# Kernel optimization log

Measured on AMD Instinct MI355X. Metric: run time of the kernel, lower is better.

## Reference

```python
import jax, jax.numpy as jnp
import numpy as np

N_NODES = 100000
N_EDGES = 1600000
IN = 128
HID = 128
EPS = 1e-5


def setup_inputs() -> dict:
    key = jax.random.key(0)
    ks = jax.random.split(key, 20)
    def lin(k, fi, fo):
        return jax.random.normal(k, (fi, fo), dtype=jnp.float32) / np.sqrt(fi)
    inp = {
        'x': jax.random.normal(ks[0], (N_NODES, IN), dtype=jnp.float32),
        'src': jax.random.randint(ks[1], (N_EDGES,), 0, N_NODES),
        'dst': jax.random.randint(ks[2], (N_EDGES,), 0, N_NODES),
        # SAGEConv layer 1..3: fc_self, fc_neigh, bias
        'Wself1': lin(ks[3], IN, HID), 'Wneigh1': lin(ks[4], IN, HID), 'b1': jnp.zeros((HID,), jnp.float32),
        'Wself2': lin(ks[5], HID, HID), 'Wneigh2': lin(ks[6], HID, HID), 'b2': jnp.zeros((HID,), jnp.float32),
        'Wself3': lin(ks[7], HID, HID), 'Wneigh3': lin(ks[8], HID, HID), 'b3': jnp.zeros((HID,), jnp.float32),
        # shared BatchNorm1d(hid)
        'gamma': jnp.ones((HID,), jnp.float32), 'beta': jnp.zeros((HID,), jnp.float32),
        # decoder MLP hid->hid->hid->1
        'Wd1': lin(ks[9], HID, HID), 'bd1': jnp.zeros((HID,), jnp.float32),
        'Wd2': lin(ks[10], HID, HID), 'bd2': jnp.zeros((HID,), jnp.float32),
        'Wd3': lin(ks[11], HID, 1), 'bd3': jnp.zeros((1,), jnp.float32),
    }
    return inp


def _sage_conv(h, src, dst, deg, Wself, Wneigh, b, n):
    # mean aggregation over in-neighbors: gather + segment-sum + divide
    neigh_sum = jax.ops.segment_sum(h[src], dst, num_segments=n)  # [N, F]
    neigh_mean = neigh_sum / deg[:, None]
    return h @ Wself + neigh_mean @ Wneigh + b


def _batch_norm(h, gamma, beta):
    mu = jnp.mean(h, axis=0)
    var = jnp.mean(jnp.square(h - mu), axis=0)  # biased var, as torch BN training
    return gamma * (h - mu) * jax.lax.rsqrt(var + EPS) + beta


def reference(x, src, dst, Wself1, Wneigh1, b1, Wself2, Wneigh2, b2,
              Wself3, Wneigh3, b3, gamma, beta, Wd1, bd1, Wd2, bd2, Wd3, bd3):
    n = x.shape[0]
    deg = jax.ops.segment_sum(jnp.ones_like(dst, dtype=x.dtype), dst, num_segments=n)
    deg = jnp.maximum(deg, 1.0)
    h = _sage_conv(x, src, dst, deg, Wself1, Wneigh1, b1, n)
    h = jax.nn.relu(_batch_norm(h, gamma, beta))  # dropout = identity (eval)
    h = _sage_conv(h, src, dst, deg, Wself2, Wneigh2, b2, n)
    h = jax.nn.relu(_batch_norm(h, gamma, beta))
    h = _sage_conv(h, src, dst, deg, Wself3, Wneigh3, b3, n)
    # decoder MLP
    h = jax.nn.relu(h @ Wd1 + bd1)
    h = jax.nn.relu(h @ Wd2 + bd2)
    return h @ Wd3 + bd3  # [N, 1]
```

## Files before the change

kernel.cpp:

```cpp
#include <hip/hip_runtime.h>

typedef unsigned short u16;
typedef unsigned int u32;
using bf16x8 = __attribute__((ext_vector_type(8))) __bf16;
using f32x4  = __attribute__((ext_vector_type(4))) float;

#define CAP 48
#define LDSROW 136

__global__ void SAGE_79328045957727_kernel() {}

__device__ __forceinline__ float bf2f(u16 u) {
  union { u32 i; float f; } v; v.i = ((u32)u) << 16; return v.f;
}
__device__ __forceinline__ u16 f2bf(float f) {
  union { float f; u32 i; } v; v.f = f;
  u32 x = v.i;
  return (u16)((x + 0x7FFFu + ((x >> 16) & 1u)) >> 16);
}


__global__ void zero_kernel(int* p, int n) {
  int i = blockIdx.x * 256 + threadIdx.x;
  if (i < n) p[i] = 0;
}


__global__ __launch_bounds__(256) void build_kernel(
    const int* __restrict__ src, const int* __restrict__ dst,
    int* __restrict__ deg, int* __restrict__ csr, int E, int npart,
    const float* __restrict__ x, u16* __restrict__ xb, long nelem4,
    const float* w0, const float* w1, const float* w2, const float* w3,
    const float* w4, const float* w5, const float* w6, const float* w7,
    u16* __restrict__ wt) {
  int b = blockIdx.x;
  if (b < 2048) {
    int p = b & 7;
    int brank = b >> 3;
    int lo = p * npart, hi = lo + npart;
    for (int i = brank * 256 + threadIdx.x; i < E; i += 256 * 256) {
      int dv = dst[i];
      if (dv >= lo && dv < hi) {
        int pos = atomicAdd(&deg[dv], 1);
        if (pos < CAP) csr[(size_t)dv * CAP + pos] = src[i];
      }
    }
  } else if (b < 2304) {
    long t = (long)(b - 2048) * 256 + threadIdx.x;
    for (long i4 = t; i4 < nelem4; i4 += 256 * 256) {
      float4 v = ((const float4*)x)[i4];
      u32* op = (u32*)(xb + i4 * 4);
      op[0] = ((u32)f2bf(v.y) << 16) | (u32)f2bf(v.x);
      op[1] = ((u32)f2bf(v.w) << 16) | (u32)f2bf(v.z);
    }
  } else {
    int tg = (b - 2304) * 256 + threadIdx.x;
    for (int k = 0; k < 8; ++k) {
      int idx = tg + k * 16384;
      int m = idx >> 14;
      int i = idx & 16383;
      const float* W = m == 0 ? w0 : m == 1 ? w1 : m == 2 ? w2 : m == 3 ? w3
                     : m == 4 ? w4 : m == 5 ? w5 : m == 6 ? w6 : w7;
      int r = i >> 7, c = i & 127;
      wt[(size_t)m * 16384 + (size_t)c * 128 + r] = f2bf(W[i]);
    }
  }
}


__global__ __launch_bounds__(256) void bnrelu_kernel(
    const u16* __restrict__ Z, u16* __restrict__ G,
    const float* __restrict__ stats, const float* __restrict__ gamma,
    const float* __restrict__ beta, long n4, float invN) {
  __shared__ float sSc[128], sSh[128];
  int t = threadIdx.x;
  if (t < 128) {
    float mu = stats[t] * invN;
    float var = stats[128 + t] * invN - mu * mu;
    float is = rsqrtf(var + 1e-5f);
    float sc = gamma[t] * is;
    sSc[t] = sc;
    sSh[t] = beta[t] - mu * sc;
  }
  __syncthreads();
  for (long i4 = (long)blockIdx.x * 256 + t; i4 < n4; i4 += (long)gridDim.x * 256) {
    uint4 q = ((const uint4*)Z)[i4];
    int c0 = ((int)(i4 & 15)) * 8;
    float e0 = fmaxf(sSc[c0+0]*bf2f((u16)(q.x & 0xffffu))+sSh[c0+0], 0.f);
    float e1 = fmaxf(sSc[c0+1]*bf2f((u16)(q.x >> 16))    +sSh[c0+1], 0.f);
    float e2 = fmaxf(sSc[c0+2]*bf2f((u16)(q.y & 0xffffu))+sSh[c0+2], 0.f);
    float e3 = fmaxf(sSc[c0+3]*bf2f((u16)(q.y >> 16))    +sSh[c0+3], 0.f);
    float e4 = fmaxf(sSc[c0+4]*bf2f((u16)(q.z & 0xffffu))+sSh[c0+4], 0.f);
    float e5 = fmaxf(sSc[c0+5]*bf2f((u16)(q.z >> 16))    +sSh[c0+5], 0.f);
    float e6 = fmaxf(sSc[c0+6]*bf2f((u16)(q.w & 0xffffu))+sSh[c0+6], 0.f);
    float e7 = fmaxf(sSc[c0+7]*bf2f((u16)(q.w >> 16))    +sSh[c0+7], 0.f);
    uint4 o;
    o.x = ((u32)f2bf(e1) << 16) | (u32)f2bf(e0);
    o.y = ((u32)f2bf(e3) << 16) | (u32)f2bf(e2);
    o.z = ((u32)f2bf(e5) << 16) | (u32)f2bf(e4);
    o.w = ((u32)f2bf(e7) << 16) | (u32)f2bf(e6);
    ((uint4*)G)[i4] = o;
  }
}


__global__ __launch_bounds__(256) void gather_kernel(
    const u16* __restrict__ G, const int* __restrict__ csr,
    const int* __restrict__ deg, u16* __restrict__ M, int N) {
  int node = blockIdx.x * 16 + (threadIdx.x >> 4);
  if (node >= N) return;
  int lane = threadIdx.x & 15;
  int fo = lane * 8;
  const int* nl = csr + (size_t)node * CAP;
  int d = deg[node];
  int dm = d < CAP ? d : CAP;
  float a0=0.f,a1=0.f,a2=0.f,a3=0.f,a4=0.f,a5=0.f,a6=0.f,a7=0.f;

#define ACC8(q) do { \
    a0 += bf2f((u16)((q).x & 0xffffu)); a1 += bf2f((u16)((q).x >> 16)); \
    a2 += bf2f((u16)((q).y & 0xffffu)); a3 += bf2f((u16)((q).y >> 16)); \
    a4 += bf2f((u16)((q).z & 0xffffu)); a5 += bf2f((u16)((q).z >> 16)); \
    a6 += bf2f((u16)((q).w & 0xffffu)); a7 += bf2f((u16)((q).w >> 16)); \
  } while (0)

  int e = 0;
  for (; e + 8 <= dm; e += 8) {
    int ia = nl[e+0], ib = nl[e+1], ic = nl[e+2], id_ = nl[e+3];
    int ie_ = nl[e+4], if_ = nl[e+5], ig = nl[e+6], ih = nl[e+7];
    uint4 q0 = *(const uint4*)(G + (size_t)ia  * 128 + fo);
    uint4 q1 = *(const uint4*)(G + (size_t)ib  * 128 + fo);
    uint4 q2 = *(const uint4*)(G + (size_t)ic  * 128 + fo);
    uint4 q3 = *(const uint4*)(G + (size_t)id_ * 128 + fo);
    uint4 q4 = *(const uint4*)(G + (size_t)ie_ * 128 + fo);
    uint4 q5 = *(const uint4*)(G + (size_t)if_ * 128 + fo);
    uint4 q6 = *(const uint4*)(G + (size_t)ig  * 128 + fo);
    uint4 q7 = *(const uint4*)(G + (size_t)ih  * 128 + fo);
    ACC8(q0); ACC8(q1); ACC8(q2); ACC8(q3);
    ACC8(q4); ACC8(q5); ACC8(q6); ACC8(q7);
  }
  if (e + 4 <= dm) {
    int ia = nl[e+0], ib = nl[e+1], ic = nl[e+2], id_ = nl[e+3];
    uint4 q0 = *(const uint4*)(G + (size_t)ia  * 128 + fo);
    uint4 q1 = *(const uint4*)(G + (size_t)ib  * 128 + fo);
    uint4 q2 = *(const uint4*)(G + (size_t)ic  * 128 + fo);
    uint4 q3 = *(const uint4*)(G + (size_t)id_ * 128 + fo);
    ACC8(q0); ACC8(q1); ACC8(q2); ACC8(q3);
    e += 4;
  }
  for (; e < dm; ++e) {
    uint4 q = *(const uint4*)(G + (size_t)nl[e] * 128 + fo);
    ACC8(q);
  }
#undef ACC8

  float inv = 1.f / (float)(d > 0 ? d : 1);
  uint4 o;
  o.x = ((u32)f2bf(a1 * inv) << 16) | (u32)f2bf(a0 * inv);
  o.y = ((u32)f2bf(a3 * inv) << 16) | (u32)f2bf(a2 * inv);
  o.z = ((u32)f2bf(a5 * inv) << 16) | (u32)f2bf(a4 * inv);
  o.w = ((u32)f2bf(a7 * inv) << 16) | (u32)f2bf(a6 * inv);
  *(uint4*)(M + (size_t)node * 128 + fo) = o;
}


__device__ __forceinline__ void stage_tile(
    const u16* __restrict__ A, u16* sT, size_t row0, int N, int tid) {
  for (int j = 0; j < 8; ++j) {
    int idx = j * 1024 + tid * 4;
    int r = idx >> 6;
    int c = idx & 63;
    size_t grow = row0 + r;
    if (grow >= (size_t)N) grow = (size_t)(N - 1);
    const u32* gp = (const u32*)(A + grow * 128) + c;
    u32 v0 = gp[0], v1 = gp[1], v2 = gp[2], v3 = gp[3];
    u32* lp = (u32*)(sT + (size_t)r * LDSROW + c * 2);
    lp[0] = v0; lp[1] = v1; lp[2] = v2; lp[3] = v3;
  }
}

__device__ __forceinline__ void mfma_tile(
    const u16* sT, const u16* __restrict__ Wt, f32x4 acc[8][2],
    int wave, int l15, int quad) {
  bf16x8 wf[2][4];
  for (int ct = 0; ct < 2; ++ct) {
    int col = wave * 32 + ct * 16 + l15;
    for (int kk = 0; kk < 4; ++kk)
      wf[ct][kk] = *(const bf16x8*)(Wt + (size_t)col * 128 + kk * 32 + quad * 8);
  }
  for (int kk = 0; kk < 4; ++kk) {
    int kbase = kk * 32 + quad * 8;
    for (int rt = 0; rt < 8; ++rt) {
      bf16x8 af = *(const bf16x8*)(sT + (size_t)(rt * 16 + l15) * LDSROW + kbase);
      acc[rt][0] = __builtin_amdgcn_mfma_f32_16x16x32_bf16(af, wf[0][kk], acc[rt][0], 0, 0, 0);
      acc[rt][1] = __builtin_amdgcn_mfma_f32_16x16x32_bf16(af, wf[1][kk], acc[rt][1], 0, 0, 0);
    }
  }
}


__global__ __launch_bounds__(256) void gemm2(
    const u16* __restrict__ A, const u16* __restrict__ B,
    const u16* __restrict__ W1t, const u16* __restrict__ W2t,
    const float* __restrict__ bias, u16* __restrict__ C,
    float* __restrict__ statsOut, int N) {
  __shared__ u16 sT[128 * LDSROW];
  int tid = threadIdx.x;
  int wave = tid >> 6;
  int lane = tid & 63;
  int l15 = lane & 15;
  int quad = lane >> 4;
  size_t row0 = (size_t)blockIdx.x * 128;

  f32x4 acc[8][2];
  for (int rt = 0; rt < 8; ++rt)
    for (int ct = 0; ct < 2; ++ct)
      for (int i = 0; i < 4; ++i) acc[rt][ct][i] = 0.f;

  stage_tile(A, sT, row0, N, tid);
  __syncthreads();
  mfma_tile(sT, W1t, acc, wave, l15, quad);
  __syncthreads();
  stage_tile(B, sT, row0, N, tid);
  __syncthreads();
  mfma_tile(sT, W2t, acc, wave, l15, quad);

  for (int ct = 0; ct < 2; ++ct) {
    int col = wave * 32 + ct * 16 + l15;
    float bv = bias[col];
    float ssum = 0.f, ssq = 0.f;
    for (int rt = 0; rt < 8; ++rt) {
      for (int i = 0; i < 4; ++i) {
        size_t row = row0 + rt * 16 + quad * 4 + i;
        if (row < (size_t)N) {
          float v = acc[rt][ct][i] + bv;
          C[row * 128 + col] = f2bf(v);
          ssum += v; ssq += v * v;
        }
      }
    }
    for (int o = 16; o < 64; o <<= 1) {
      ssum += __shfl_xor(ssum, o);
      ssq  += __shfl_xor(ssq, o);
    }
    if (quad == 0) {
      atomicAdd(&statsOut[col], ssum);
      atomicAdd(&statsOut[128 + col], ssq);
    }
  }
}


__global__ __launch_bounds__(256) void megagemm(
    const u16* __restrict__ G, const u16* __restrict__ M,
    const u16* __restrict__ wtS3, const u16* __restrict__ wtN3,
    const float* __restrict__ b3,
    const u16* __restrict__ wtD1, const float* __restrict__ bd1,
    const u16* __restrict__ wtD2, const float* __restrict__ bd2,
    const float* __restrict__ wd3, const float* __restrict__ bd3,
    float* __restrict__ outF, int N) {
  __shared__ u16 sT[128 * LDSROW];
  __shared__ float sOut[128];

  int tid = threadIdx.x;
  int wave = tid >> 6;
  int lane = tid & 63;
  int l15 = lane & 15;
  int quad = lane >> 4;
  size_t row0 = (size_t)blockIdx.x * 128;

  if (tid < 128) sOut[tid] = 0.f;

  f32x4 acc[8][2];
  for (int rt = 0; rt < 8; ++rt)
    for (int ct = 0; ct < 2; ++ct)
      for (int i = 0; i < 4; ++i) acc[rt][ct][i] = 0.f;

  stage_tile(M, sT, row0, N, tid);
  __syncthreads();
  mfma_tile(sT, wtN3, acc, wave, l15, quad);
  __syncthreads();
  stage_tile(G, sT, row0, N, tid);
  __syncthreads();
  mfma_tile(sT, wtS3, acc, wave, l15, quad);

  for (int g = 0; g < 2; ++g) {
    const u16* Wt = g ? wtD2 : wtD1;
    const float* bs = g ? bd1 : b3;
    int do_relu = g;

    __syncthreads();
    for (int ct = 0; ct < 2; ++ct) {
      int col = wave * 32 + ct * 16 + l15;
      float bv = bs[col];
      for (int rt = 0; rt < 8; ++rt) {
        for (int i = 0; i < 4; ++i) {
          int row = rt * 16 + quad * 4 + i;
          float v = acc[rt][ct][i] + bv;
          if (do_relu) v = fmaxf(v, 0.f);
          sT[(size_t)row * LDSROW + col] = f2bf(v);
        }
      }
    }
    __syncthreads();

    for (int rt = 0; rt < 8; ++rt)
      for (int ct = 0; ct < 2; ++ct)
        for (int i = 0; i < 4; ++i) acc[rt][ct][i] = 0.f;
    mfma_tile(sT, Wt, acc, wave, l15, quad);
  }

  {
    int col0 = wave * 32 + l15;
    float bv0 = bd2[col0], bv1 = bd2[col0 + 16];
    float w30 = wd3[col0], w31 = wd3[col0 + 16];
    for (int rt = 0; rt < 8; ++rt) {
      for (int i = 0; i < 4; ++i) {
        size_t row = row0 + rt * 16 + quad * 4 + i;
        float v0 = fmaxf(acc[rt][0][i] + bv0, 0.f);
        float v1 = fmaxf(acc[rt][1][i] + bv1, 0.f);
        float pv = v0 * w30 + v1 * w31;
        pv += __shfl_xor(pv, 1);
        pv += __shfl_xor(pv, 2);
        pv += __shfl_xor(pv, 4);
        pv += __shfl_xor(pv, 8);
        if (l15 == 0 && row < (size_t)N)
          atomicAdd(&sOut[rt * 16 + quad * 4 + i], pv);
      }
    }
    __syncthreads();
    if (tid < 128) {
      size_t row = row0 + tid;
      if (row < (size_t)N) outF[row] = sOut[tid] + bd3[0];
    }
  }
}


extern "C" void kernel_launch(void* const* d_in, const int* in_sizes, int n_in,
                              void* d_out, int out_size, void* d_ws, size_t ws_size,
                              hipStream_t stream) {
  const float* x      = (const float*)d_in[0];
  const int*   src    = (const int*)d_in[1];
  const int*   dst    = (const int*)d_in[2];
  const float* Wself1 = (const float*)d_in[3];
  const float* Wneigh1= (const float*)d_in[4];
  const float* b1     = (const float*)d_in[5];
  const float* Wself2 = (const float*)d_in[6];
  const float* Wneigh2= (const float*)d_in[7];
  const float* b2     = (const float*)d_in[8];
  const float* Wself3 = (const float*)d_in[9];
  const float* Wneigh3= (const float*)d_in[10];
  const float* b3     = (const float*)d_in[11];
  const float* gamma  = (const float*)d_in[12];
  const float* beta   = (const float*)d_in[13];
  const float* Wd1    = (const float*)d_in[14];
  const float* bd1    = (const float*)d_in[15];
  const float* Wd2    = (const float*)d_in[16];
  const float* bd2    = (const float*)d_in[17];
  const float* Wd3    = (const float*)d_in[18];
  const float* bd3    = (const float*)d_in[19];
  float* out = (float*)d_out;

  int N = in_sizes[0] / 128;
  int E = in_sizes[1];
  int npart = (N + 7) / 8;

  char* ws = (char*)d_ws;
  size_t off = 0;
  int* deg; int* csr; float* stats1; float* stats2;
  u16* xb; u16* ZA; u16* ZB; u16* M; u16* wt;
  deg   = (int*)(ws + off);   off += (size_t)N * 4;
  stats1= (float*)(ws + off); off += 256 * 4;
  stats2= (float*)(ws + off); off += 256 * 4;
  off = (off + 511) & ~(size_t)511;
  csr  = (int*)(ws + off);   off += ((size_t)N * CAP * 4 + 511) & ~(size_t)511;
  wt   = (u16*)(ws + off);   off += ((size_t)8 * 16384 * 2 + 511) & ~(size_t)511;
  xb   = (u16*)(ws + off);   off += ((size_t)N * 128 * 2 + 511) & ~(size_t)511;
  ZA   = (u16*)(ws + off);   off += ((size_t)N * 128 * 2 + 511) & ~(size_t)511;
  ZB   = (u16*)(ws + off);   off += ((size_t)N * 128 * 2 + 511) & ~(size_t)511;
  M    = (u16*)(ws + off);   off += ((size_t)N * 128 * 2 + 511) & ~(size_t)511;

  u16* wtS1 = wt + 0 * 16384; u16* wtN1 = wt + 1 * 16384;
  u16* wtS2 = wt + 2 * 16384; u16* wtN2 = wt + 3 * 16384;
  u16* wtS3 = wt + 4 * 16384; u16* wtN3 = wt + 5 * 16384;
  u16* wtD1 = wt + 6 * 16384; u16* wtD2 = wt + 7 * 16384;

  zero_kernel<<<(N + 512 + 255) / 256, 256, 0, stream>>>(deg, N + 512);

  long nelem4 = (long)N * 128 / 4;
  build_kernel<<<2368, 256, 0, stream>>>(
      src, dst, deg, csr, E, npart, x, xb, nelem4,
      Wself1, Wneigh1, Wself2, Wneigh2, Wself3, Wneigh3, Wd1, Wd2, wt);

  int strips = (N + 127) / 128;
  int g16    = (N + 15) / 16;
  float invN = 1.f / (float)N;
  long n4 = (long)N * 16;

  gather_kernel<<<g16, 256, 0, stream>>>(xb, csr, deg, M, N);
  gemm2<<<strips, 256, 0, stream>>>(xb, M, wtS1, wtN1, b1, ZA, stats1, N);

  bnrelu_kernel<<<2048, 256, 0, stream>>>(ZA, ZA, stats1, gamma, beta, n4, invN);

  gather_kernel<<<g16, 256, 0, stream>>>(ZA, csr, deg, M, N);
  gemm2<<<strips, 256, 0, stream>>>(ZA, M, wtS2, wtN2, b2, ZB, stats2, N);

  bnrelu_kernel<<<2048, 256, 0, stream>>>(ZB, ZB, stats2, gamma, beta, n4, invN);

  gather_kernel<<<g16, 256, 0, stream>>>(ZB, csr, deg, M, N);
  megagemm<<<strips, 256, 0, stream>>>(
      ZB, M, wtS3, wtN3, b3, wtD1, bd1, wtD2, bd2, Wd3, bd3, out, N);
}
```

Before: 564.8 us.

## Prefetch second GEMM operand into registers and simplify CSR build partitioning

The two-operand GEMM kernels now load the second input tile into registers before the first MFMA pass, so its global reads overlap with compute instead of being issued after a barrier. The CSR build no longer makes 8 partitioned passes over the edge list that each filter by destination range. Every edge is now handled once with an atomic insert, which cuts redundant reads of dst but gives up the partition's locality of atomics. The register prefetch adds 32 VGPRs per thread, which may lower occupancy.

New measurement: 557.2 us. No clear change (-1.3%).

```diff
diff --git a/kernel.cpp b/kernel.cpp
--- a/kernel.cpp
+++ b/kernel.cpp
@@ -28,25 +28,20 @@
 
 __global__ __launch_bounds__(256) void build_kernel(
     const int* __restrict__ src, const int* __restrict__ dst,
-    int* __restrict__ deg, int* __restrict__ csr, int E, int npart,
+    int* __restrict__ deg, int* __restrict__ csr, int E,
     const float* __restrict__ x, u16* __restrict__ xb, long nelem4,
     const float* w0, const float* w1, const float* w2, const float* w3,
     const float* w4, const float* w5, const float* w6, const float* w7,
     u16* __restrict__ wt) {
   int b = blockIdx.x;
-  if (b < 2048) {
-    int p = b & 7;
-    int brank = b >> 3;
-    int lo = p * npart, hi = lo + npart;
-    for (int i = brank * 256 + threadIdx.x; i < E; i += 256 * 256) {
+  if (b < 1024) {
+    for (int i = b * 256 + threadIdx.x; i < E; i += 1024 * 256) {
       int dv = dst[i];
-      if (dv >= lo && dv < hi) {
-        int pos = atomicAdd(&deg[dv], 1);
-        if (pos < CAP) csr[(size_t)dv * CAP + pos] = src[i];
-      }
-    }
-  } else if (b < 2304) {
-    long t = (long)(b - 2048) * 256 + threadIdx.x;
+      int pos = atomicAdd(&deg[dv], 1);
+      if (pos < CAP) csr[(size_t)dv * CAP + pos] = src[i];
+    }
+  } else if (b < 1280) {
+    long t = (long)(b - 1024) * 256 + threadIdx.x;
     for (long i4 = t; i4 < nelem4; i4 += 256 * 256) {
       float4 v = ((const float4*)x)[i4];
       u32* op = (u32*)(xb + i4 * 4);
@@ -54,7 +49,7 @@
       op[1] = ((u32)f2bf(v.w) << 16) | (u32)f2bf(v.z);
     }
   } else {
-    int tg = (b - 2304) * 256 + threadIdx.x;
+    int tg = (b - 1280) * 256 + threadIdx.x;
     for (int k = 0; k < 8; ++k) {
       int idx = tg + k * 16384;
       int m = idx >> 14;
@@ -178,6 +173,30 @@
   }
 }
 
+__device__ __forceinline__ void preload_tile(
+    const u16* __restrict__ A, u32 rb[8][4], size_t row0, int N, int tid) {
+  for (int j = 0; j < 8; ++j) {
+    int idx = j * 1024 + tid * 4;
+    int r = idx >> 6;
+    int c = idx & 63;
+    size_t grow = row0 + r;
+    if (grow >= (size_t)N) grow = (size_t)(N - 1);
+    const u32* gp = (const u32*)(A + grow * 128) + c;
+    rb[j][0] = gp[0]; rb[j][1] = gp[1]; rb[j][2] = gp[2]; rb[j][3] = gp[3];
+  }
+}
+
+__device__ __forceinline__ void write_tile(
+    const u32 rb[8][4], u16* sT, int tid) {
+  for (int j = 0; j < 8; ++j) {
+    int idx = j * 1024 + tid * 4;
+    int r = idx >> 6;
+    int c = idx & 63;
+    u32* lp = (u32*)(sT + (size_t)r * LDSROW + c * 2);
+    lp[0] = rb[j][0]; lp[1] = rb[j][1]; lp[2] = rb[j][2]; lp[3] = rb[j][3];
+  }
+}
+
 __device__ __forceinline__ void mfma_tile(
     const u16* sT, const u16* __restrict__ Wt, f32x4 acc[8][2],
     int wave, int l15, int quad) {
@@ -216,11 +235,13 @@
     for (int ct = 0; ct < 2; ++ct)
       for (int i = 0; i < 4; ++i) acc[rt][ct][i] = 0.f;
 
+  u32 rb[8][4];
+  preload_tile(B, rb, row0, N, tid);
   stage_tile(A, sT, row0, N, tid);
   __syncthreads();
   mfma_tile(sT, W1t, acc, wave, l15, quad);
   __syncthreads();
-  stage_tile(B, sT, row0, N, tid);
+  write_tile(rb, sT, tid);
   __syncthreads();
   mfma_tile(sT, W2t, acc, wave, l15, quad);
 
@@ -275,11 +296,13 @@
     for (int ct = 0; ct < 2; ++ct)
       for (int i = 0; i < 4; ++i) acc[rt][ct][i] = 0.f;
 
+  u32 rb[8][4];
+  preload_tile(G, rb, row0, N, tid);
   stage_tile(M, sT, row0, N, tid);
   __syncthreads();
   mfma_tile(sT, wtN3, acc, wave, l15, quad);
   __syncthreads();
-  stage_tile(G, sT, row0, N, tid);
+  write_tile(rb, sT, tid);
   __syncthreads();
   mfma_tile(sT, wtS3, acc, wave, l15, quad);
 
@@ -363,7 +386,6 @@
 
   int N = in_sizes[0] / 128;
   int E = in_sizes[1];
-  int npart = (N + 7) / 8;
 
   char* ws = (char*)d_ws;
   size_t off = 0;
@@ -388,8 +410,8 @@
   zero_kernel<<<(N + 512 + 255) / 256, 256, 0, stream>>>(deg, N + 512);
 
   long nelem4 = (long)N * 128 / 4;
-  build_kernel<<<2368, 256, 0, stream>>>(
-      src, dst, deg, csr, E, npart, x, xb, nelem4,
+  build_kernel<<<1344, 256, 0, stream>>>(
+      src, dst, deg, csr, E, x, xb, nelem4,
       Wself1, Wneigh1, Wself2, Wneigh2, Wself3, Wneigh3, Wd1, Wd2, wt);
 
   int strips = (N + 127) / 128;
```
